# Kernel tuning notes

Measured on AMD Instinct MI355X. Metric: run time of the kernel, lower is better.

## Reference

```python
import jax, jax.numpy as jnp
import numpy as np

NEG_SLOPE = 0.2

def gat_layer(x, src, dst, W, a_src, a_dst, num_nodes):
    """PyG-style GATConv. W:[F_in,H*C], a_src/a_dst:[H,C]. Returns [N,H,C]."""
    H, C = a_src.shape
    h = (x @ W).reshape(num_nodes, H, C)                      # [N,H,C]
    e_src = jnp.sum(h * a_src, axis=-1)                       # [N,H]
    e_dst = jnp.sum(h * a_dst, axis=-1)                       # [N,H]
    e = jax.nn.leaky_relu(e_src[src] + e_dst[dst], NEG_SLOPE) # [E,H]
    # segment softmax over incoming edges of each destination node
    m = jax.ops.segment_max(e, dst, num_segments=num_nodes)
    w = jnp.exp(e - m[dst])
    z = jax.ops.segment_sum(w, dst, num_segments=num_nodes)
    alpha = w / (z[dst] + 1e-16)                               # [E,H]
    msg = h[src] * alpha[:, :, None]                           # [E,H,C]
    return jax.ops.segment_sum(msg, dst, num_segments=num_nodes)


def setup_inputs() -> dict:
    key = jax.random.key(0)
    ks = jax.random.split(key, 16)
    N, E, F_IN, HID, A, G = 50000, 800000, 128, 128, 32, 64
    x = jax.random.normal(ks[0], (N, F_IN), dtype=jnp.float32)
    edge_index = jax.random.randint(ks[1], (2, E), 0, N, dtype=jnp.int32)
    batch = jnp.sort(jax.random.randint(ks[2], (N,), 0, G, dtype=jnp.int32))
    s = 0.1
    W1 = jax.random.normal(ks[3], (F_IN, 2 * HID), jnp.float32) * s
    a_src1 = jax.random.normal(ks[4], (2, HID), jnp.float32) * s
    a_dst1 = jax.random.normal(ks[5], (2, HID), jnp.float32) * s
    b1 = jnp.zeros((2 * HID,), jnp.float32)
    W2 = jax.random.normal(ks[6], (2 * HID, HID), jnp.float32) * s
    a_src2 = jax.random.normal(ks[7], (1, HID), jnp.float32) * s
    a_dst2 = jax.random.normal(ks[8], (1, HID), jnp.float32) * s
    b2 = jnp.zeros((HID,), jnp.float32)
    Wp = jax.random.normal(ks[9], (HID, A), jnp.float32) * s
    bp = jnp.zeros((A,), jnp.float32)
    Wv = jax.random.normal(ks[10], (HID, 1), jnp.float32) * s
    bv = jnp.zeros((1,), jnp.float32)
    return {"x": x, "edge_index": edge_index, "batch": batch,
            "W1": W1, "a_src1": a_src1, "a_dst1": a_dst1, "b1": b1,
            "W2": W2, "a_src2": a_src2, "a_dst2": a_dst2, "b2": b2,
            "Wp": Wp, "bp": bp, "Wv": Wv, "bv": bv}


def reference(x, edge_index, batch, W1, a_src1, a_dst1, b1,
              W2, a_src2, a_dst2, b2, Wp, bp, Wv, bv):
    N = x.shape[0]
    G = 64  # number of graphs in the batch
    # add self-loops (PyG GATConv default)
    loop = jnp.arange(N, dtype=edge_index.dtype)
    src = jnp.concatenate([edge_index[0], loop])
    dst = jnp.concatenate([edge_index[1], loop])
    # layer 1: heads=2, concat=True
    h1 = gat_layer(x, src, dst, W1, a_src1, a_dst1, N)        # [N,2,HID]
    h1 = jax.nn.elu(h1.reshape(N, -1) + b1)                   # [N,2*HID]
    # layer 2: heads=1, concat=False (mean over heads = identity for H=1)
    h2 = gat_layer(h1, src, dst, W2, a_src2, a_dst2, N)       # [N,1,HID]
    h2 = jax.nn.elu(h2.reshape(N, -1) + b2)                   # [N,HID]
    # global mean pool over graphs
    sums = jax.ops.segment_sum(h2, batch, num_segments=G)
    cnt = jax.ops.segment_sum(jnp.ones((N,), h2.dtype), batch, num_segments=G)
    x_pool = sums / jnp.maximum(cnt, 1.0)[:, None]            # [G,HID]
    policy_logits = x_pool @ Wp + bp                          # [G,A]
    state_value = x_pool @ Wv + bv                            # [G,1]
    return (policy_logits, state_value)
```

## Files before the change

kernel.cpp:

```cpp
#include <hip/hip_runtime.h>
#include <hip/hip_bf16.h>
#include <cstdint>


typedef __attribute__((ext_vector_type(8))) short bf16x8;
typedef __attribute__((ext_vector_type(4))) float f32x4;

#define NBLK_H 160
#define BSH 6
#define BMSK 63

__device__ __forceinline__ float wave_sum(float v) {
#pragma unroll
    for (int off = 32; off >= 1; off >>= 1) v += __shfl_xor(v, off, 64);
    return v;
}

__device__ __forceinline__ unsigned short f2bf(float f) {
    union { float f; uint32_t u; } c; c.f = f;
    uint32_t u = c.u;
    return (unsigned short)((u + 0x7fffu + ((u >> 16) & 1u)) >> 16);
}

__device__ __forceinline__ float bf2f(unsigned short u) {
    union { uint32_t u; float f; } c; c.u = ((uint32_t)u) << 16;
    return c.f;
}


template <int K, int FOUT>
__device__ __forceinline__ void swizzle_body(const float* __restrict__ W, int ldW, int colOff,
                                             unsigned short* __restrict__ Bsw, int tid) {
    constexpr int CPW = FOUT / 4, NCT = CPW / 16, KST = K / 32;
    if (tid >= K * FOUT / 8) return;
    int lane = tid & 63;
    int rest = tid >> 6;
    int t = rest % KST; rest /= KST;
    int c = rest % NCT; rest /= NCT;
    int cg_ = rest;
    int quad = lane >> 4, lo = lane & 15;
    int col = colOff + cg_ * CPW + c * 16 + lo;
    unsigned short v[8];
#pragma unroll
    for (int j = 0; j < 8; ++j)
        v[j] = f2bf(W[(t * 32 + quad * 8 + j) * ldW + col]);
    ushort4* dst = (ushort4*)(Bsw + (size_t)tid * 8);
    ushort4 o0, o1;
    o0.x = v[0]; o0.y = v[1]; o0.z = v[2]; o0.w = v[3];
    o1.x = v[4]; o1.y = v[5]; o1.z = v[6]; o1.w = v[7];
    dst[0] = o0; dst[1] = o1;
}


__global__ __launch_bounds__(256) void init_kernel(
        const float* __restrict__ W1, const float* __restrict__ W2,
        const float* __restrict__ a_src1, const float* __restrict__ a_dst1,
        unsigned short* __restrict__ B1h0, unsigned short* __restrict__ B1h1,
        unsigned short* __restrict__ B2,
        float* __restrict__ v1s, float* __restrict__ v1d,
        int* __restrict__ zbase, int zn4, int ZB,
        const int* __restrict__ ei, int* __restrict__ hist,
        int E, int ET, int CHUNK, int NB) {
    __shared__ int bins[1024];
    int b = blockIdx.x;
    if (b < 8)        swizzle_body<128, 128>(W1, 256, 0,   B1h0, b * 256 + threadIdx.x);
    else if (b < 16)  swizzle_body<128, 128>(W1, 256, 128, B1h1, (b - 8) * 256 + threadIdx.x);
    else if (b < 32)  swizzle_body<256, 128>(W2, 128, 0,   B2, (b - 16) * 256 + threadIdx.x);
    else if (b == 32) {
        int t = threadIdx.x, h = t >> 7, k = t & 127;
        float vs = 0.f, vd = 0.f;
        for (int c = 0; c < 128; ++c) {
            float w = W1[k * 256 + h * 128 + c];
            vs += w * a_src1[h * 128 + c];
            vd += w * a_dst1[h * 128 + c];
        }
        v1s[h * 128 + k] = vs;
        v1d[h * 128 + k] = vd;
    } else if (b < 33 + ZB) {
        int i = (b - 33) * 256 + threadIdx.x;
        if (i < zn4) ((int4*)zbase)[i] = make_int4(0, 0, 0, 0);
    } else {
        const int blk = b - 33 - ZB;
        for (int t = threadIdx.x; t < NB; t += 256) bins[t] = 0;
        __syncthreads();
        const int start = blk * CHUNK, end = min(ET, start + CHUNK);
        for (int i = start + threadIdx.x; i < end; i += 256) {
            int dst = (i < E) ? ei[E + i] : (i - E);
            atomicAdd(&bins[dst >> BSH], 1);
        }
        __syncthreads();
        for (int t = threadIdx.x; t < NB; t += 256) hist[t * NBLK_H + blk] = bins[t];
    }
}


__global__ __launch_bounds__(256) void scan_attn1(
        int* __restrict__ hist, int* __restrict__ tsum, int M, int TILESH,
        const float* __restrict__ x, const float* __restrict__ v1s,
        const float* __restrict__ v1d, float* __restrict__ es1,
        float* __restrict__ ed1, unsigned short* __restrict__ xbf, int N) {
    __shared__ int buf[256];
    if ((int)blockIdx.x < TILESH) {
        const int t = threadIdx.x;
        const int base = blockIdx.x * 1024 + t * 4;
        int v[4]; int s = 0;
#pragma unroll
        for (int k = 0; k < 4; ++k) { v[k] = (base + k < M) ? hist[base + k] : 0; s += v[k]; }
        buf[t] = s;
        __syncthreads();
#pragma unroll
        for (int off = 1; off < 256; off <<= 1) {
            int xx = (t >= off) ? buf[t - off] : 0;
            __syncthreads();
            buf[t] += xx;
            __syncthreads();
        }
        int run = buf[t] - s;
#pragma unroll
        for (int k = 0; k < 4; ++k) {
            if (base + k < M) hist[base + k] = run;
            run += v[k];
        }
        if (t == 255) tsum[blockIdx.x] = buf[255];
        return;
    }
    int bid = blockIdx.x - TILESH;
    int wid = (bid * 256 + threadIdx.x) >> 6;
    int lane = threadIdx.x & 63;
    if (wid >= N) return;
    float2 xv = *(const float2*)(x + (size_t)wid * 128 + lane * 2);
    float p0s = xv.x * v1s[lane * 2] + xv.y * v1s[lane * 2 + 1];
    float p1s = xv.x * v1s[128 + lane * 2] + xv.y * v1s[128 + lane * 2 + 1];
    float p0d = xv.x * v1d[lane * 2] + xv.y * v1d[lane * 2 + 1];
    float p1d = xv.x * v1d[128 + lane * 2] + xv.y * v1d[128 + lane * 2 + 1];
    p0s = wave_sum(p0s); p1s = wave_sum(p1s);
    p0d = wave_sum(p0d); p1d = wave_sum(p1d);
    if (lane == 0) {
        es1[wid * 2] = p0s; es1[wid * 2 + 1] = p1s;
        ed1[wid * 2] = p0d; ed1[wid * 2 + 1] = p1d;
    }
    ushort2 o; o.x = f2bf(xv.x); o.y = f2bf(xv.y);
    *(ushort2*)(xbf + (size_t)wid * 128 + lane * 2) = o;
}

__global__ __launch_bounds__(256) void scan_add(const int* __restrict__ partial,
                                                const int* __restrict__ tsum,
                                                int* __restrict__ out, int M, int T) {
    __shared__ int sb[256];
    const int t = threadIdx.x;
    sb[t] = (t < T) ? tsum[t] : 0;
    __syncthreads();
#pragma unroll
    for (int off = 1; off < 256; off <<= 1) {
        int v = (t >= off) ? sb[t - off] : 0;
        __syncthreads();
        sb[t] += v;
        __syncthreads();
    }
    const int tile = blockIdx.x;
    if (tile == 0 && t == 0) out[M] = sb[255];
    const int toff = (tile == 0) ? 0 : sb[tile - 1];
    int i = tile * 1024 + t * 4;
#pragma unroll
    for (int k = 0; k < 4; ++k) {
        if (i + k < M) out[i + k] = partial[i + k] + toff;
    }
}

__global__ __launch_bounds__(256) void part_kernel(const int* __restrict__ ei,
                                                   const int* __restrict__ histscan,
                                                   int* __restrict__ bsorted,
                                                   int E, int ET, int CHUNK, int NB) {
    __shared__ int scur[1024];
    const int blk = blockIdx.x;
    for (int t = threadIdx.x; t < NB; t += 256) scur[t] = histscan[t * NBLK_H + blk];
    __syncthreads();
    const int start = blk * CHUNK, end = min(ET, start + CHUNK);
    for (int i = start + threadIdx.x; i < end; i += 256) {
        int dst = (i < E) ? ei[E + i] : (i - E);
        int src = (i < E) ? ei[i] : dst;
        int pos = atomicAdd(&scur[dst >> BSH], 1);
        bsorted[pos] = (src << BSH) | (dst & BMSK);
    }
}

__global__ __launch_bounds__(256) void bucket_kernel(const int* __restrict__ bsorted,
                                                     const int* __restrict__ histscan,
                                                     int* __restrict__ csr_src,
                                                     int* __restrict__ rowptr,
                                                     int N, int NB) {
    __shared__ int cnt[64];
    __shared__ int excl[64];
    __shared__ int ebuf[2304];
    const int b = blockIdx.x;
    const int gbase = histscan[b * NBLK_H];
    const int gend  = histscan[(b + 1) * NBLK_H];
    const int sz = gend - gbase;
    const int t = threadIdx.x;
    if (b == 0 && t == 255) rowptr[N] = histscan[NB * NBLK_H];
    if (t < 64) cnt[t] = 0;
    __syncthreads();
    const bool fits = (sz <= 2304);
    if (fits) {
        for (int i = t; i < sz; i += 256) {
            int p = bsorted[gbase + i];
            ebuf[i] = p;
            atomicAdd(&cnt[p & BMSK], 1);
        }
    } else {
        for (int i = t; i < sz; i += 256) {
            int p = bsorted[gbase + i];
            atomicAdd(&cnt[p & BMSK], 1);
        }
    }
    __syncthreads();
    if (t < 64) excl[t] = cnt[t];
    __syncthreads();
    for (int off = 1; off < 64; off <<= 1) {
        int v = (t < 64 && t >= off) ? excl[t - off] : 0;
        __syncthreads();
        if (t < 64) excl[t] += v;
        __syncthreads();
    }
    if (t < 64) {
        int dst = (b << BSH) + t;
        if (dst < N) rowptr[dst] = gbase + excl[t] - cnt[t];
    }
    __syncthreads();
    if (t < 64) cnt[t] = excl[t] - cnt[t];
    __syncthreads();
    if (fits) {
        for (int i = t; i < sz; i += 256) {
            int p = ebuf[i];
            int pos = atomicAdd(&cnt[p & BMSK], 1);
            csr_src[gbase + pos] = p >> BSH;
        }
    } else {
        for (int i = t; i < sz; i += 256) {
            int p = bsorted[gbase + i];
            int pos = atomicAdd(&cnt[p & BMSK], 1);
            csr_src[gbase + pos] = p >> BSH;
        }
    }
}


#define ACC2(U_, WW_, P_, Q_) { float v_;                              \
    v_ = bf2f(U_.x); P_.x += WW_.x * v_; Q_.x += WW_.y * v_;           \
    v_ = bf2f(U_.y); P_.y += WW_.x * v_; Q_.y += WW_.y * v_;           \
    v_ = bf2f(U_.z); P_.z += WW_.x * v_; Q_.z += WW_.y * v_;           \
    v_ = bf2f(U_.w); P_.w += WW_.x * v_; Q_.w += WW_.y * v_; }

__global__ void gat_agg_x(const unsigned short* __restrict__ xbf,
                          const float* __restrict__ es, const float* __restrict__ ed,
                          const int* __restrict__ rowptr, const int* __restrict__ csr_src,
                          unsigned short* __restrict__ aggx, int N, int NPAD) {
    __shared__ float2 w_lds[4][32];
    __shared__ int    s_lds[4][32];
    int wid = (blockIdx.x * blockDim.x + threadIdx.x) >> 6;
    int lane = threadIdx.x & 63;
    if (wid >= N) return;
    const int wave = threadIdx.x >> 6;
    const int rs = rowptr[wid], re = rowptr[wid + 1];
    const int half = lane >> 5, c = lane & 31;
    const float edn = ed[wid * 2 + half];

    float z = 0.f;
    float4 p0 = {0.f, 0.f, 0.f, 0.f}, p1 = {0.f, 0.f, 0.f, 0.f};
    float4 q0 = {0.f, 0.f, 0.f, 0.f}, q1 = {0.f, 0.f, 0.f, 0.f};
    for (int i = rs; i < re; i += 32) {
        const int cnt = min(re - i, 32);
        if (c < cnt) {
            int s = csr_src[i + c];
            float e = es[s * 2 + half] + edn;
            e = (e > 0.f) ? e : 0.2f * e;
            float ww = __expf(e);
            ((float*)&w_lds[wave][c])[half] = ww;
            if (half == 0) s_lds[wave][c] = s;
            z += ww;
        }
        int k = half;
        for (; k + 14 < cnt; k += 16) {
            int s0 = s_lds[wave][k + 0],  s1 = s_lds[wave][k + 2];
            int s2 = s_lds[wave][k + 4],  s3 = s_lds[wave][k + 6];
            int s4 = s_lds[wave][k + 8],  s5 = s_lds[wave][k + 10];
            int s6 = s_lds[wave][k + 12], s7 = s_lds[wave][k + 14];
            float2 wv0 = w_lds[wave][k + 0],  wv1 = w_lds[wave][k + 2];
            float2 wv2 = w_lds[wave][k + 4],  wv3 = w_lds[wave][k + 6];
            float2 wv4 = w_lds[wave][k + 8],  wv5 = w_lds[wave][k + 10];
            float2 wv6 = w_lds[wave][k + 12], wv7 = w_lds[wave][k + 14];
            ushort4 u0 = *(const ushort4*)(xbf + (size_t)s0 * 128 + c * 4);
            ushort4 u1 = *(const ushort4*)(xbf + (size_t)s1 * 128 + c * 4);
            ushort4 u2 = *(const ushort4*)(xbf + (size_t)s2 * 128 + c * 4);
            ushort4 u3 = *(const ushort4*)(xbf + (size_t)s3 * 128 + c * 4);
            ushort4 u4 = *(const ushort4*)(xbf + (size_t)s4 * 128 + c * 4);
            ushort4 u5 = *(const ushort4*)(xbf + (size_t)s5 * 128 + c * 4);
            ushort4 u6 = *(const ushort4*)(xbf + (size_t)s6 * 128 + c * 4);
            ushort4 u7 = *(const ushort4*)(xbf + (size_t)s7 * 128 + c * 4);
            ACC2(u0, wv0, p0, q0);
            ACC2(u1, wv1, p1, q1);
            ACC2(u2, wv2, p0, q0);
            ACC2(u3, wv3, p1, q1);
            ACC2(u4, wv4, p0, q0);
            ACC2(u5, wv5, p1, q1);
            ACC2(u6, wv6, p0, q0);
            ACC2(u7, wv7, p1, q1);
        }
        for (; k + 6 < cnt; k += 8) {
            int s0 = s_lds[wave][k + 0], s1 = s_lds[wave][k + 2];
            int s2 = s_lds[wave][k + 4], s3 = s_lds[wave][k + 6];
            float2 wv0 = w_lds[wave][k + 0], wv1 = w_lds[wave][k + 2];
            float2 wv2 = w_lds[wave][k + 4], wv3 = w_lds[wave][k + 6];
            ushort4 u0 = *(const ushort4*)(xbf + (size_t)s0 * 128 + c * 4);
            ushort4 u1 = *(const ushort4*)(xbf + (size_t)s1 * 128 + c * 4);
            ushort4 u2 = *(const ushort4*)(xbf + (size_t)s2 * 128 + c * 4);
            ushort4 u3 = *(const ushort4*)(xbf + (size_t)s3 * 128 + c * 4);
            ACC2(u0, wv0, p0, q0);
            ACC2(u1, wv1, p1, q1);
            ACC2(u2, wv2, p0, q0);
            ACC2(u3, wv3, p1, q1);
        }
        for (; k < cnt; k += 2) {
            int s0 = s_lds[wave][k];
            float2 wv = w_lds[wave][k];
            ushort4 u0 = *(const ushort4*)(xbf + (size_t)s0 * 128 + c * 4);
            ACC2(u0, wv, p0, q0);
        }
    }
#pragma unroll
    for (int off = 16; off >= 1; off >>= 1) z += __shfl_xor(z, off, 64);
    const float rz = 1.f / (z + 1e-16f);
    float4 p, q;
    p.x = p0.x + p1.x; p.y = p0.y + p1.y; p.z = p0.z + p1.z; p.w = p0.w + p1.w;
    q.x = q0.x + q1.x; q.y = q0.y + q1.y; q.z = q0.z + q1.z; q.w = q0.w + q1.w;
    p.x += __shfl_xor(p.x, 32, 64); p.y += __shfl_xor(p.y, 32, 64);
    p.z += __shfl_xor(p.z, 32, 64); p.w += __shfl_xor(p.w, 32, 64);
    q.x += __shfl_xor(q.x, 32, 64); q.y += __shfl_xor(q.y, 32, 64);
    q.z += __shfl_xor(q.z, 32, 64); q.w += __shfl_xor(q.w, 32, 64);
    float ox = (half ? q.x : p.x) * rz;
    float oy = (half ? q.y : p.y) * rz;
    float oz = (half ? q.z : p.z) * rz;
    float ow = (half ? q.w : p.w) * rz;
    ushort4 o;
    o.x = f2bf(ox); o.y = f2bf(oy); o.z = f2bf(oz); o.w = f2bf(ow);
    *(ushort4*)(aggx + ((size_t)half * NPAD + wid) * 128 + c * 4) = o;
}


__global__ __launch_bounds__(256) void gemm12_fused(
        const unsigned short* __restrict__ Abase,
        const unsigned short* __restrict__ B1h0, const unsigned short* __restrict__ B1h1,
        const unsigned short* __restrict__ B2sw,
        const float* __restrict__ b1,
        const float* __restrict__ a_src, const float* __restrict__ a_dst,
        float* __restrict__ es, float* __restrict__ ed,
        unsigned short* __restrict__ C, int N, int NPAD) {
    __shared__ unsigned short h1t[64][264];
    __shared__ float lds_ps[4][64];
    __shared__ float lds_pd[4][64];
    const int tid = threadIdx.x;
    const int wave = tid >> 6, lane = tid & 63;
    const int quad = lane >> 4, lo = lane & 15;
    const int n0 = blockIdx.x * 64;

    {
        const int head = wave >> 1, wh = wave & 1;
        const unsigned short* A = Abase + (size_t)head * NPAD * 128;
        const bf16x8* Bp = (const bf16x8*)(head ? B1h1 : B1h0);
        bf16x8 bf[4][4];
#pragma unroll
        for (int c = 0; c < 4; ++c)
#pragma unroll
            for (int t = 0; t < 4; ++t)
                bf[c][t] = Bp[((wh * 4 + c) * 4 + t) * 64 + lane];
        f32x4 acc[4][4];
#pragma unroll
        for (int r = 0; r < 4; ++r)
#pragma unroll
            for (int c = 0; c < 4; ++c) acc[r][c] = (f32x4){0.f, 0.f, 0.f, 0.f};
#pragma unroll
        for (int r = 0; r < 4; ++r) {
            const unsigned short* Ar = A + (size_t)(n0 + r * 16 + lo) * 128 + quad * 8;
#pragma unroll
            for (int t = 0; t < 4; ++t) {
                bf16x8 af = *(const bf16x8*)(Ar + t * 32);
#pragma unroll
                for (int c = 0; c < 4; ++c)
                    acc[r][c] = __builtin_amdgcn_mfma_f32_16x16x32_bf16(af, bf[c][t],
                                                                       acc[r][c], 0, 0, 0);
            }
        }
#pragma unroll
        for (int r = 0; r < 4; ++r) {
            int rl = r * 16 + quad * 4;
#pragma unroll
            for (int c = 0; c < 4; ++c) {
                int col = head * 128 + wh * 64 + c * 16 + lo;
                float bv = b1[col];
#pragma unroll
                for (int j = 0; j < 4; ++j) {
                    float v = acc[r][c][j] + bv;
                    v = (v > 0.f) ? v : __expf(v) - 1.f;
                    h1t[rl + j][col] = f2bf(v);
                }
            }
        }
    }
    __syncthreads();

    bf16x8 bf2[2][8];
    {
        const bf16x8* Bp2 = (const bf16x8*)B2sw;
#pragma unroll
        for (int c = 0; c < 2; ++c)
#pragma unroll
            for (int t = 0; t < 8; ++t)
                bf2[c][t] = Bp2[((wave * 2 + c) * 8 + t) * 64 + lane];
    }
    f32x4 acc2[4][2];
#pragma unroll
    for (int r = 0; r < 4; ++r)
#pragma unroll
        for (int c = 0; c < 2; ++c) acc2[r][c] = (f32x4){0.f, 0.f, 0.f, 0.f};
#pragma unroll
    for (int r = 0; r < 4; ++r) {
        const unsigned short* Ar = &h1t[r * 16 + lo][quad * 8];
#pragma unroll
        for (int t = 0; t < 8; ++t) {
            bf16x8 af = *(const bf16x8*)(Ar + t * 32);
#pragma unroll
            for (int c = 0; c < 2; ++c)
                acc2[r][c] = __builtin_amdgcn_mfma_f32_16x16x32_bf16(af, bf2[c][t],
                                                                    acc2[r][c], 0, 0, 0);
        }
    }
    const int c0 = wave * 32;
#pragma unroll
    for (int r = 0; r < 4; ++r) {
        int row = n0 + r * 16 + quad * 4;
#pragma unroll
        for (int c = 0; c < 2; ++c) {
            int col = c0 + c * 16 + lo;
#pragma unroll
            for (int j = 0; j < 4; ++j)
                if (row + j < N) C[(size_t)(row + j) * 128 + col] = f2bf(acc2[r][c][j]);
        }
    }
    float asv[2], adv[2];
#pragma unroll
    for (int c = 0; c < 2; ++c) {
        int col = c0 + c * 16 + lo;
        asv[c] = a_src[col];
        adv[c] = a_dst[col];
    }
#pragma unroll
    for (int r = 0; r < 4; ++r) {
#pragma unroll
        for (int j = 0; j < 4; ++j) {
            float ps = 0.f, pd = 0.f;
#pragma unroll
            for (int c = 0; c < 2; ++c) { ps += acc2[r][c][j] * asv[c]; pd += acc2[r][c][j] * adv[c]; }
#pragma unroll
            for (int off = 1; off <= 8; off <<= 1) {
                ps += __shfl_xor(ps, off, 64);
                pd += __shfl_xor(pd, off, 64);
            }
            if (lo == 0) {
                int row_l = r * 16 + quad * 4 + j;
                lds_ps[wave][row_l] = ps;
                lds_pd[wave][row_l] = pd;
            }
        }
    }
    __syncthreads();
    if (tid < 64) {
        int row = tid;
        int n = n0 + row;
        if (n < N) {
            es[n] = lds_ps[0][row] + lds_ps[1][row] + lds_ps[2][row] + lds_ps[3][row];
            ed[n] = lds_pd[0][row] + lds_pd[1][row] + lds_pd[2][row] + lds_pd[3][row];
        }
    }
}


__global__ void gat_agg_h1(const unsigned short* __restrict__ Hpre,
                           const float* __restrict__ es, const float* __restrict__ ed,
                           const int* __restrict__ rowptr, const int* __restrict__ csr_src,
                           const float* __restrict__ bias, unsigned short* __restrict__ out,
                           int N) {
    __shared__ float w_lds[4][64];
    __shared__ int   s_lds[4][64];
    int wid = (blockIdx.x * blockDim.x + threadIdx.x) >> 6;
    int lane = threadIdx.x & 63;
    if (wid >= N) return;
    const int wave = threadIdx.x >> 6;
    const int rs = rowptr[wid], re = rowptr[wid + 1];
    const int half = lane >> 5, c = lane & 31;
    const float edn = ed[wid];

    float z = 0.f;
    float4 a0 = {0.f, 0.f, 0.f, 0.f}, a1 = {0.f, 0.f, 0.f, 0.f};
    float4 a2 = {0.f, 0.f, 0.f, 0.f}, a3 = {0.f, 0.f, 0.f, 0.f};
    for (int i = rs; i < re; i += 64) {
        const int cnt = min(re - i, 64);
        if (lane < cnt) {
            int s = csr_src[i + lane];
            float e = es[s] + edn;
            e = (e > 0.f) ? e : 0.2f * e;
            float ww = __expf(e);
            w_lds[wave][lane] = ww;
            s_lds[wave][lane] = s;
            z += ww;
        }
        int k = half;
        for (; k + 14 < cnt; k += 16) {
            int s0 = s_lds[wave][k],      s1 = s_lds[wave][k + 2];
            int s2 = s_lds[wave][k + 4],  s3 = s_lds[wave][k + 6];
            int s4 = s_lds[wave][k + 8],  s5 = s_lds[wave][k + 10];
            int s6 = s_lds[wave][k + 12], s7 = s_lds[wave][k + 14];
            float w0 = w_lds[wave][k],      w1 = w_lds[wave][k + 2];
            float w2 = w_lds[wave][k + 4],  w3 = w_lds[wave][k + 6];
            float w4 = w_lds[wave][k + 8],  w5 = w_lds[wave][k + 10];
            float w6 = w_lds[wave][k + 12], w7 = w_lds[wave][k + 14];
            ushort4 u0 = *(const ushort4*)(Hpre + (size_t)s0 * 128 + c * 4);
            ushort4 u1 = *(const ushort4*)(Hpre + (size_t)s1 * 128 + c * 4);
            ushort4 u2 = *(const ushort4*)(Hpre + (size_t)s2 * 128 + c * 4);
            ushort4 u3 = *(const ushort4*)(Hpre + (size_t)s3 * 128 + c * 4);
            ushort4 u4 = *(const ushort4*)(Hpre + (size_t)s4 * 128 + c * 4);
            ushort4 u5 = *(const ushort4*)(Hpre + (size_t)s5 * 128 + c * 4);
            ushort4 u6 = *(const ushort4*)(Hpre + (size_t)s6 * 128 + c * 4);
            ushort4 u7 = *(const ushort4*)(Hpre + (size_t)s7 * 128 + c * 4);
            a0.x += w0 * bf2f(u0.x); a0.y += w0 * bf2f(u0.y);
            a0.z += w0 * bf2f(u0.z); a0.w += w0 * bf2f(u0.w);
            a1.x += w1 * bf2f(u1.x); a1.y += w1 * bf2f(u1.y);
            a1.z += w1 * bf2f(u1.z); a1.w += w1 * bf2f(u1.w);
            a2.x += w2 * bf2f(u2.x); a2.y += w2 * bf2f(u2.y);
            a2.z += w2 * bf2f(u2.z); a2.w += w2 * bf2f(u2.w);
            a3.x += w3 * bf2f(u3.x); a3.y += w3 * bf2f(u3.y);
            a3.z += w3 * bf2f(u3.z); a3.w += w3 * bf2f(u3.w);
            a0.x += w4 * bf2f(u4.x); a0.y += w4 * bf2f(u4.y);
            a0.z += w4 * bf2f(u4.z); a0.w += w4 * bf2f(u4.w);
            a1.x += w5 * bf2f(u5.x); a1.y += w5 * bf2f(u5.y);
            a1.z += w5 * bf2f(u5.z); a1.w += w5 * bf2f(u5.w);
            a2.x += w6 * bf2f(u6.x); a2.y += w6 * bf2f(u6.y);
            a2.z += w6 * bf2f(u6.z); a2.w += w6 * bf2f(u6.w);
            a3.x += w7 * bf2f(u7.x); a3.y += w7 * bf2f(u7.y);
            a3.z += w7 * bf2f(u7.z); a3.w += w7 * bf2f(u7.w);
        }
        for (; k + 6 < cnt; k += 8) {
            int s0 = s_lds[wave][k], s1 = s_lds[wave][k + 2];
            int s2 = s_lds[wave][k + 4], s3 = s_lds[wave][k + 6];
            float w0 = w_lds[wave][k], w1 = w_lds[wave][k + 2];
            float w2 = w_lds[wave][k + 4], w3 = w_lds[wave][k + 6];
            ushort4 u0 = *(const ushort4*)(Hpre + (size_t)s0 * 128 + c * 4);
            ushort4 u1 = *(const ushort4*)(Hpre + (size_t)s1 * 128 + c * 4);
            ushort4 u2 = *(const ushort4*)(Hpre + (size_t)s2 * 128 + c * 4);
            ushort4 u3 = *(const ushort4*)(Hpre + (size_t)s3 * 128 + c * 4);
            a0.x += w0 * bf2f(u0.x); a0.y += w0 * bf2f(u0.y);
            a0.z += w0 * bf2f(u0.z); a0.w += w0 * bf2f(u0.w);
            a1.x += w1 * bf2f(u1.x); a1.y += w1 * bf2f(u1.y);
            a1.z += w1 * bf2f(u1.z); a1.w += w1 * bf2f(u1.w);
            a2.x += w2 * bf2f(u2.x); a2.y += w2 * bf2f(u2.y);
            a2.z += w2 * bf2f(u2.z); a2.w += w2 * bf2f(u2.w);
            a3.x += w3 * bf2f(u3.x); a3.y += w3 * bf2f(u3.y);
            a3.z += w3 * bf2f(u3.z); a3.w += w3 * bf2f(u3.w);
        }
        for (; k < cnt; k += 2) {
            int s0 = s_lds[wave][k];
            float w0 = w_lds[wave][k];
            ushort4 u0 = *(const ushort4*)(Hpre + (size_t)s0 * 128 + c * 4);
            a0.x += w0 * bf2f(u0.x); a0.y += w0 * bf2f(u0.y);
            a0.z += w0 * bf2f(u0.z); a0.w += w0 * bf2f(u0.w);
        }
    }
    z = wave_sum(z);
    const float rz = 1.f / (z + 1e-16f);

    float ox = a0.x + a1.x + a2.x + a3.x;
    float oy = a0.y + a1.y + a2.y + a3.y;
    float oz = a0.z + a1.z + a2.z + a3.z;
    float ow = a0.w + a1.w + a2.w + a3.w;
    ox += __shfl_xor(ox, 32, 64);
    oy += __shfl_xor(oy, 32, 64);
    oz += __shfl_xor(oz, 32, 64);
    ow += __shfl_xor(ow, 32, 64);
    if (lane < 32) {
        float4 bv = ((const float4*)bias)[c];
        ox = ox * rz + bv.x; oy = oy * rz + bv.y; oz = oz * rz + bv.z; ow = ow * rz + bv.w;
        ox = (ox > 0.f) ? ox : __expf(ox) - 1.f;
        oy = (oy > 0.f) ? oy : __expf(oy) - 1.f;
        oz = (oz > 0.f) ? oz : __expf(oz) - 1.f;
        ow = (ow > 0.f) ? ow : __expf(ow) - 1.f;
        ushort4 o;
        o.x = f2bf(ox); o.y = f2bf(oy); o.z = f2bf(oz); o.w = f2bf(ow);
        *(ushort4*)(out + (size_t)wid * 128 + c * 4) = o;
    }
}


#define PCHUNK 256

__global__ __launch_bounds__(256) void pool_partial(const unsigned short* __restrict__ h2,
                                                    const int* __restrict__ batch,
                                                    float* __restrict__ xsum,
                                                    int* __restrict__ cnt, int N) {
    const int base = blockIdx.x * PCHUNK;
    const int rg = threadIdx.x >> 6;
    const int c2 = threadIdx.x & 63;
    float ax = 0.f, ay = 0.f;
    int gcur = -1, run = 0;
    for (int r = rg; r < PCHUNK; r += 4) {
        int i = base + r;
        if (i >= N) break;
        int g = batch[i];
        if (g != gcur) {
            if (gcur >= 0) {
                atomicAdd(&xsum[gcur * 128 + c2 * 2 + 0], ax);
                atomicAdd(&xsum[gcur * 128 + c2 * 2 + 1], ay);
                if (c2 == 0) atomicAdd(&cnt[gcur], run);
            }
            gcur = g; ax = 0.f; ay = 0.f; run = 0;
        }
        ushort2 u = *(const ushort2*)(h2 + (size_t)i * 128 + c2 * 2);
        ax += bf2f(u.x); ay += bf2f(u.y);
        run += 1;
    }
    if (gcur >= 0) {
        atomicAdd(&xsum[gcur * 128 + c2 * 2 + 0], ax);
        atomicAdd(&xsum[gcur * 128 + c2 * 2 + 1], ay);
        if (c2 == 0) atomicAdd(&cnt[gcur], run);
    }
}


__global__ void head_kernel(const float* __restrict__ xsum, const int* __restrict__ cnt,
                            const float* __restrict__ Wp, const float* __restrict__ bp,
                            const float* __restrict__ Wv, const float* __restrict__ bv,
                            float* __restrict__ out) {
    int g = blockIdx.x, t = threadIdx.x;
    __shared__ float p[128];
    float inv = 1.f / fmaxf((float)cnt[g], 1.f);
    p[t] = xsum[g * 128 + t] * inv;
    p[t + 64] = xsum[g * 128 + t + 64] * inv;
    __syncthreads();
    if (t < 32) {
        float acc = bp[t];
        for (int k = 0; k < 128; ++k) acc += p[k] * Wp[k * 32 + t];
        out[g * 32 + t] = acc;
    } else if (t == 32) {
        float acc = bv[0];
        for (int k = 0; k < 128; ++k) acc += p[k] * Wv[k];
        out[64 * 32 + g] = acc;
    }
}


extern "C" void kernel_launch(void* const* d_in, const int* in_sizes, int n_in,
                              void* d_out, int out_size, void* d_ws, size_t ws_size,
                              hipStream_t stream) {
    const float* x      = (const float*)d_in[0];
    const int*   ei     = (const int*)d_in[1];
    const int*   batch  = (const int*)d_in[2];
    const float* W1     = (const float*)d_in[3];
    const float* a_src1 = (const float*)d_in[4];
    const float* a_dst1 = (const float*)d_in[5];
    const float* b1     = (const float*)d_in[6];
    const float* W2     = (const float*)d_in[7];
    const float* a_src2 = (const float*)d_in[8];
    const float* a_dst2 = (const float*)d_in[9];
    const float* b2     = (const float*)d_in[10];
    const float* Wp     = (const float*)d_in[11];
    const float* bp     = (const float*)d_in[12];
    const float* Wv     = (const float*)d_in[13];
    const float* bv     = (const float*)d_in[14];

    const int N  = in_sizes[0] / 128;
    const int E  = in_sizes[1] / 2;
    const int ET = E + N;
    const int NPAD = ((N + 63) / 64) * 64;
    const int NBLK = NPAD / 64;
    const int PBLK = (N + PCHUNK - 1) / PCHUNK;
    const int NB = (N + 63) >> BSH;
    const int CHUNK = (ET + NBLK_H - 1) / NBLK_H;
    const int M = NB * NBLK_H;
    const int TILESH = (M + 1023) / 1024;
    const int AB = (N + 3) / 4;

    char* ws = (char*)d_ws;
    size_t off = 0;
    auto alloc = [&](size_t bytes) -> void* {
        void* p = ws + off;
        off = (off + bytes + 255) & ~(size_t)255;
        return p;
    };
    unsigned short* xbf   = (unsigned short*)alloc((size_t)NPAD * 128 * 2);
    unsigned short* aggx  = (unsigned short*)alloc((size_t)2 * NPAD * 128 * 2);
    unsigned short* h2pre = (unsigned short*)alloc((size_t)NPAD * 128 * 2);
    unsigned short* h2bf  = (unsigned short*)alloc((size_t)N * 128 * 2);
    unsigned short* w1h0  = (unsigned short*)alloc((size_t)128 * 128 * 2);
    unsigned short* w1h1  = (unsigned short*)alloc((size_t)128 * 128 * 2);
    unsigned short* w2sw  = (unsigned short*)alloc((size_t)256 * 128 * 2);
    float* v1s = (float*)alloc(256 * 4);
    float* v1d = (float*)alloc(256 * 4);
    float* es1 = (float*)alloc((size_t)N * 2 * 4);
    float* ed1 = (float*)alloc((size_t)N * 2 * 4);
    float* es2 = (float*)alloc((size_t)N * 4);
    float* ed2 = (float*)alloc((size_t)N * 4);
    const int ZINTS = 64 * 128 + 64;
    int*   zbase  = (int*)alloc(((size_t)ZINTS + 8) * 4);
    float* xsum   = (float*)zbase;
    int*   cnt    = (int*)(xsum + 64 * 128);
    int*   rowptr   = (int*)alloc((size_t)(N + 1) * 4);
    int*   hist     = (int*)alloc((size_t)M * 4);
    int*   histscan = (int*)alloc((size_t)(M + 1) * 4);
    int*   bsorted  = (int*)alloc((size_t)ET * 4);
    int*   csrsrc   = (int*)alloc((size_t)ET * 4);
    int*   tsum     = (int*)alloc(256 * 4);
    const int zn4 = (ZINTS + 3) / 4;
    const int ZB = (zn4 + 255) / 256;

    init_kernel<<<33 + ZB + NBLK_H, 256, 0, stream>>>(W1, W2, a_src1, a_dst1,
                                                      w1h0, w1h1, w2sw, v1s, v1d,
                                                      zbase, zn4, ZB,
                                                      ei, hist, E, ET, CHUNK, NB);
    scan_attn1<<<TILESH + AB, 256, 0, stream>>>(hist, tsum, M, TILESH,
                                                x, v1s, v1d, es1, ed1, xbf, N);
    scan_add<<<TILESH, 256, 0, stream>>>(hist, tsum, histscan, M, TILESH);
    part_kernel<<<NBLK_H, 256, 0, stream>>>(ei, histscan, bsorted, E, ET, CHUNK, NB);
    bucket_kernel<<<NB, 256, 0, stream>>>(bsorted, histscan, csrsrc, rowptr, N, NB);
    gat_agg_x<<<(N + 3) / 4, 256, 0, stream>>>(xbf, es1, ed1, rowptr, csrsrc, aggx, N, NPAD);
    gemm12_fused<<<NBLK, 256, 0, stream>>>(aggx, w1h0, w1h1, w2sw, b1,
                                           a_src2, a_dst2, es2, ed2, h2pre, N, NPAD);
    gat_agg_h1<<<(N + 3) / 4, 256, 0, stream>>>(h2pre, es2, ed2, rowptr, csrsrc, b2,
                                                h2bf, N);
    pool_partial<<<PBLK, 256, 0, stream>>>(h2bf, batch, xsum, cnt, N);
    head_kernel<<<64, 64, 0, stream>>>(xsum, cnt, Wp, bp, Wv, bv, (float*)d_out);
}
```

Baseline: 291.5 us.

## Fold scan_add into part_kernel and drop 16-wide unroll in gat_agg_x

Each part_kernel block now computes the tile-offset scan from tsum itself and adds it to the raw histogram on the fly, which removes the separate scan_add launch and the full histscan array. Block 0 writes a compact segbase array (one entry per bucket) that bucket_kernel reads instead of strided histscan entries. Separately, the 16-edge unrolled gather loop in the layer-1 aggregation is removed, leaving the 8-wide loop, which may lower register pressure but reduces memory-level parallelism. Every part block repeats the small 256-element scan, which is redundant work.

```diff
diff --git a/kernel.cpp b/kernel.cpp
--- a/kernel.cpp
+++ b/kernel.cpp
@@ -9,6 +9,7 @@
 #define NBLK_H 160
 #define BSH 6
 #define BMSK 63
+#define PCHUNK 256
 
 __device__ __forceinline__ float wave_sum(float v) {
 #pragma unroll
@@ -143,10 +144,15 @@
     *(ushort2*)(xbf + (size_t)wid * 128 + lane * 2) = o;
 }
 
-__global__ __launch_bounds__(256) void scan_add(const int* __restrict__ partial,
-                                                const int* __restrict__ tsum,
-                                                int* __restrict__ out, int M, int T) {
+
+__global__ __launch_bounds__(256) void part_kernel(const int* __restrict__ ei,
+                                                   const int* __restrict__ hist,
+                                                   const int* __restrict__ tsum,
+                                                   int* __restrict__ bsorted,
+                                                   int* __restrict__ segbase,
+                                                   int E, int ET, int CHUNK, int NB, int T) {
     __shared__ int sb[256];
+    __shared__ int scur[1024];
     const int t = threadIdx.x;
     sb[t] = (t < T) ? tsum[t] : 0;
     __syncthreads();
@@ -157,26 +163,18 @@
         sb[t] += v;
         __syncthreads();
     }
-    const int tile = blockIdx.x;
-    if (tile == 0 && t == 0) out[M] = sb[255];
-    const int toff = (tile == 0) ? 0 : sb[tile - 1];
-    int i = tile * 1024 + t * 4;
-#pragma unroll
-    for (int k = 0; k < 4; ++k) {
-        if (i + k < M) out[i + k] = partial[i + k] + toff;
-    }
-}
-
-__global__ __launch_bounds__(256) void part_kernel(const int* __restrict__ ei,
-                                                   const int* __restrict__ histscan,
-                                                   int* __restrict__ bsorted,
-                                                   int E, int ET, int CHUNK, int NB) {
-    __shared__ int scur[1024];
     const int blk = blockIdx.x;
-    for (int t = threadIdx.x; t < NB; t += 256) scur[t] = histscan[t * NBLK_H + blk];
+    for (int b = t; b < NB; b += 256) {
+        int idx = b * NBLK_H + blk;
+        int tile = idx >> 10;
+        int v = hist[idx] + (tile ? sb[tile - 1] : 0);
+        scur[b] = v;
+        if (blk == 0) segbase[b] = v;
+    }
+    if (blk == 0 && t == 0) segbase[NB] = sb[T - 1];
     __syncthreads();
     const int start = blk * CHUNK, end = min(ET, start + CHUNK);
-    for (int i = start + threadIdx.x; i < end; i += 256) {
+    for (int i = start + t; i < end; i += 256) {
         int dst = (i < E) ? ei[E + i] : (i - E);
         int src = (i < E) ? ei[i] : dst;
         int pos = atomicAdd(&scur[dst >> BSH], 1);
@@ -184,8 +182,9 @@
     }
 }
 
+
 __global__ __launch_bounds__(256) void bucket_kernel(const int* __restrict__ bsorted,
-                                                     const int* __restrict__ histscan,
+                                                     const int* __restrict__ segbase,
                                                      int* __restrict__ csr_src,
                                                      int* __restrict__ rowptr,
                                                      int N, int NB) {
@@ -193,11 +192,11 @@
     __shared__ int excl[64];
     __shared__ int ebuf[2304];
     const int b = blockIdx.x;
-    const int gbase = histscan[b * NBLK_H];
-    const int gend  = histscan[(b + 1) * NBLK_H];
+    const int gbase = segbase[b];
+    const int gend  = segbase[b + 1];
     const int sz = gend - gbase;
     const int t = threadIdx.x;
-    if (b == 0 && t == 255) rowptr[N] = histscan[NB * NBLK_H];
+    if (b == 0 && t == 255) rowptr[N] = segbase[NB];
     if (t < 64) cnt[t] = 0;
     __syncthreads();
     const bool fits = (sz <= 2304);
@@ -280,32 +279,6 @@
             z += ww;
         }
         int k = half;
-        for (; k + 14 < cnt; k += 16) {
-            int s0 = s_lds[wave][k + 0],  s1 = s_lds[wave][k + 2];
-            int s2 = s_lds[wave][k + 4],  s3 = s_lds[wave][k + 6];
-            int s4 = s_lds[wave][k + 8],  s5 = s_lds[wave][k + 10];
-            int s6 = s_lds[wave][k + 12], s7 = s_lds[wave][k + 14];
-            float2 wv0 = w_lds[wave][k + 0],  wv1 = w_lds[wave][k + 2];
-            float2 wv2 = w_lds[wave][k + 4],  wv3 = w_lds[wave][k + 6];
-            float2 wv4 = w_lds[wave][k + 8],  wv5 = w_lds[wave][k + 10];
-            float2 wv6 = w_lds[wave][k + 12], wv7 = w_lds[wave][k + 14];
-            ushort4 u0 = *(const ushort4*)(xbf + (size_t)s0 * 128 + c * 4);
-            ushort4 u1 = *(const ushort4*)(xbf + (size_t)s1 * 128 + c * 4);
-            ushort4 u2 = *(const ushort4*)(xbf + (size_t)s2 * 128 + c * 4);
-            ushort4 u3 = *(const ushort4*)(xbf + (size_t)s3 * 128 + c * 4);
-            ushort4 u4 = *(const ushort4*)(xbf + (size_t)s4 * 128 + c * 4);
-            ushort4 u5 = *(const ushort4*)(xbf + (size_t)s5 * 128 + c * 4);
-            ushort4 u6 = *(const ushort4*)(xbf + (size_t)s6 * 128 + c * 4);
-            ushort4 u7 = *(const ushort4*)(xbf + (size_t)s7 * 128 + c * 4);
-            ACC2(u0, wv0, p0, q0);
-            ACC2(u1, wv1, p1, q1);
-            ACC2(u2, wv2, p0, q0);
-            ACC2(u3, wv3, p1, q1);
-            ACC2(u4, wv4, p0, q0);
-            ACC2(u5, wv5, p1, q1);
-            ACC2(u6, wv6, p0, q0);
-            ACC2(u7, wv7, p1, q1);
-        }
         for (; k + 6 < cnt; k += 8) {
             int s0 = s_lds[wave][k + 0], s1 = s_lds[wave][k + 2];
             int s2 = s_lds[wave][k + 4], s3 = s_lds[wave][k + 6];
@@ -599,8 +572,6 @@
 }
 
 
-#define PCHUNK 256
-
 __global__ __launch_bounds__(256) void pool_partial(const unsigned short* __restrict__ h2,
                                                     const int* __restrict__ batch,
                                                     float* __restrict__ xsum,
@@ -711,12 +682,12 @@
     int*   zbase  = (int*)alloc(((size_t)ZINTS + 8) * 4);
     float* xsum   = (float*)zbase;
     int*   cnt    = (int*)(xsum + 64 * 128);
-    int*   rowptr   = (int*)alloc((size_t)(N + 1) * 4);
-    int*   hist     = (int*)alloc((size_t)M * 4);
-    int*   histscan = (int*)alloc((size_t)(M + 1) * 4);
-    int*   bsorted  = (int*)alloc((size_t)ET * 4);
-    int*   csrsrc   = (int*)alloc((size_t)ET * 4);
-    int*   tsum     = (int*)alloc(256 * 4);
+    int*    rowptr    = (int*)alloc((size_t)(N + 1) * 4);
+    int*    hist      = (int*)alloc((size_t)M * 4);
+    int*    segbase   = (int*)alloc((size_t)(NB + 1) * 4);
+    int*    bsorted   = (int*)alloc((size_t)ET * 4);
+    int*    csrsrc    = (int*)alloc((size_t)ET * 4);
+    int*    tsum      = (int*)alloc(256 * 4);
     const int zn4 = (ZINTS + 3) / 4;
     const int ZB = (zn4 + 255) / 256;
 
@@ -726,9 +697,9 @@
                                                       ei, hist, E, ET, CHUNK, NB);
     scan_attn1<<<TILESH + AB, 256, 0, stream>>>(hist, tsum, M, TILESH,
                                                 x, v1s, v1d, es1, ed1, xbf, N);
-    scan_add<<<TILESH, 256, 0, stream>>>(hist, tsum, histscan, M, TILESH);
-    part_kernel<<<NBLK_H, 256, 0, stream>>>(ei, histscan, bsorted, E, ET, CHUNK, NB);
-    bucket_kernel<<<NB, 256, 0, stream>>>(bsorted, histscan, csrsrc, rowptr, N, NB);
+    part_kernel<<<NBLK_H, 256, 0, stream>>>(ei, hist, tsum, bsorted, segbase,
+                                            E, ET, CHUNK, NB, TILESH);
+    bucket_kernel<<<NB, 256, 0, stream>>>(bsorted, segbase, csrsrc, rowptr, N, NB);
     gat_agg_x<<<(N + 3) / 4, 256, 0, stream>>>(xbf, es1, ed1, rowptr, csrsrc, aggx, N, NPAD);
     gemm12_fused<<<NBLK, 256, 0, stream>>>(aggx, w1h0, w1h1, w2sw, b1,
                                            a_src2, a_dst2, es2, ed2, h2pre, N, NPAD);
```

New measurement: 283.8 us. 1.03x faster.
